# Kernel optimization log

Hardware: AMD Instinct MI355X
Metric: run time of the kernel (lower is better)

Reference implementation:

```python
import jax, jax.numpy as jnp
import numpy as np

TEMPERATURE = 0.07

def _l2norm(x):
    return x / jnp.linalg.norm(x, axis=-1, keepdims=True)

def setup_inputs() -> dict:
    key = jax.random.key(0)
    k1, k2, k3, k4 = jax.random.split(key, 4)
    B, T, C_ctx, C_enc, P, K = 8, 256, 512, 256, 12, 128
    context = jax.random.normal(k1, (B, T, C_ctx), dtype=jnp.float32)
    encoded = jax.random.normal(k2, (B, T, C_enc), dtype=jnp.float32)
    W = jax.random.normal(k3, (P, C_enc, C_ctx), dtype=jnp.float32) * (1.0 / np.sqrt(C_ctx))
    neg_idx = jax.random.randint(k4, (P, B * (T - 1), K), 0, B * T, dtype=jnp.int64)
    return {"context": context, "encoded": encoded, "W": W, "neg_idx": neg_idx}

def reference(context, encoded, W, neg_idx):
    B, T, C_enc = encoded.shape
    n_pred = W.shape[0]
    # normalized pool of all encoded vectors [B*T, C_enc]
    pool = _l2norm(encoded.reshape(B * T, C_enc))
    total = jnp.float32(0.0)
    for k in range(1, n_pred + 1):  # fixed small loop over horizons
        Nk = B * (T - k)
        c_t = context[:, : T - k, :]                       # [B, T-k, C_ctx]
        z_hat = jnp.einsum('btc,ec->bte', c_t, W[k - 1])   # [B, T-k, C_enc]
        z_hat = _l2norm(z_hat.reshape(Nk, C_enc))
        z_pos = _l2norm(encoded[:, k:, :].reshape(Nk, C_enc))
        pos_logits = jnp.sum(z_hat * z_pos, axis=-1, keepdims=True)  # [Nk, 1]
        z_neg = pool[neg_idx[k - 1, :Nk]]                  # [Nk, K, C_enc]
        neg_logits = jnp.einsum('nc,nkc->nk', z_hat, z_neg)
        logits = jnp.concatenate([pos_logits, neg_logits], axis=1) / TEMPERATURE
        # cross-entropy with target class 0
        step_loss = jnp.mean(jax.nn.logsumexp(logits, axis=-1) - logits[:, 0])
        total = total + step_loss
    return total / n_pred
```

## Files before the change

### kernel.cpp

```cpp
#include <hip/hip_runtime.h>
#include <hip/hip_bf16.h>

typedef __attribute__((ext_vector_type(8))) short short8;
typedef __attribute__((ext_vector_type(4))) float f32x4;
typedef _Float16 __attribute__((ext_vector_type(2))) half2v;

#define INV_TEMP 14.285714285714286f
#define LOGIT_MAX 14.2857143f
#define L2E 1.44269504f
#define OFFE (LOGIT_MAX * L2E)
#define PCLIP 0.23f
#define PDELTA (PCLIP / 7.f)
#define PQS (7.f / PCLIP)

__device__ __forceinline__ ushort bf16c(float f) {
  uint u = __float_as_uint(f);
  uint r = (u + 0x7fffu + ((u >> 16) & 1u)) >> 16;
  return (ushort)r;
}
__device__ __forceinline__ uint pk2(float a, float b) {
  return (uint)bf16c(a) | ((uint)bf16c(b) << 16);
}
__device__ __forceinline__ uint pkh(float a, float b) {
  return __builtin_bit_cast(uint, __builtin_amdgcn_cvt_pkrtz(a, b));
}
__device__ __forceinline__ half2v h2(uint u) {
  return __builtin_bit_cast(half2v, u);
}
__device__ __forceinline__ int sdot4_(uint a, uint b, int c) {
  return __builtin_amdgcn_sdot4((int)a, (int)b, c, false);
}
__device__ __forceinline__ void gl_lds16(const void* g, void* l) {
  __builtin_amdgcn_global_load_lds(
      (const __attribute__((address_space(1))) void*)g,
      (__attribute__((address_space(3))) void*)l, 16, 0, 0);
}

template <int CTRL>
__device__ __forceinline__ float dpp_add(float v) {
  const int x = __builtin_amdgcn_mov_dpp(__float_as_int(v), CTRL, 0xF, 0xF, true);
  return v + __int_as_float(x);
}
template <int CTRL>
__device__ __forceinline__ int dpp_addi(int v) {
  return v + __builtin_amdgcn_mov_dpp(v, CTRL, 0xF, 0xF, true);
}
__device__ __forceinline__ float qsum16(float v) {
  v = dpp_add<0xB1>(v);
  v = dpp_add<0x4E>(v);
  v = dpp_add<0x141>(v);
  v = dpp_add<0x140>(v);
  return v;
}
__device__ __forceinline__ int qsum8i(int v) {
  v = dpp_addi<0xB1>(v);
  v = dpp_addi<0x4E>(v);
  v = dpp_addi<0x141>(v);
  return v;
}

__global__ __launch_bounds__(256) void prep_kernel(
    const float* __restrict__ ctx, const float* __restrict__ W,
    const float* __restrict__ enc, ushort* __restrict__ ctxb,
    ushort* __restrict__ Wb, uint* __restrict__ pool4,
    float* __restrict__ acc) {
  const int bid = blockIdx.x;
  const int tid = threadIdx.x;
  if (bid < 1280) {
    const float* in;
    ushort* out;
    size_t i;
    if (bid < 512) { in = ctx; out = ctxb; i = (size_t)bid * 256 + tid; }
    else           { in = W;   out = Wb;   i = (size_t)(bid - 512) * 256 + tid; }
    const float4 a = *(const float4*)(in + i * 8);
    const float4 b = *(const float4*)(in + i * 8 + 4);
    const uint4 o = make_uint4(pk2(a.x, a.y), pk2(a.z, a.w), pk2(b.x, b.y), pk2(b.z, b.w));
    *(uint4*)(out + i * 8) = o;
    return;
  }
  if (bid == 1280 && tid < 12) acc[tid] = 0.f;
  const int grp = tid >> 4, lane = tid & 15;
  const int r = (bid - 1280) * 16 + grp;
  const float* src = enc + (size_t)r * 256 + lane * 16;
  float4 v0 = *(const float4*)(src);
  float4 v1 = *(const float4*)(src + 4);
  float4 v2 = *(const float4*)(src + 8);
  float4 v3 = *(const float4*)(src + 12);
  float c[16] = {v0.x, v0.y, v0.z, v0.w, v1.x, v1.y, v1.z, v1.w,
                 v2.x, v2.y, v2.z, v2.w, v3.x, v3.y, v3.z, v3.w};
  float ss = 0.f;
#pragma unroll
  for (int i = 0; i < 16; ++i) ss = fmaf(c[i], c[i], ss);
  ss = qsum16(ss);
  const float qs = rsqrtf(ss) * PQS;
  uint w0 = 0, w1 = 0;
#pragma unroll
  for (int n = 0; n < 8; ++n) {
    const int q0 = (int)rintf(fminf(fmaxf(c[n] * qs, -7.f), 7.f)) + 8;
    const int q1 = (int)rintf(fminf(fmaxf(c[8 + n] * qs, -7.f), 7.f)) + 8;
    w0 |= (uint)q0 << (4 * n);
    w1 |= (uint)q1 << (4 * n);
  }
  *(uint2*)(pool4 + (size_t)r * 32 + lane * 2) = make_uint2(w0, w1);
}

__global__ __launch_bounds__(256) void zhat_gemm_kernel(
    const ushort* __restrict__ ctxb, const ushort* __restrict__ Wb,
    uint* __restrict__ Zp) {
  const int kk = blockIdx.z;
  const int Tk = 255 - kk, Nk = 8 * Tk;
  const int rowbase = blockIdx.y * 64;
  if (rowbase >= Nk) return;
  const int colbase = blockIdx.x * 128;

  __shared__ __attribute__((aligned(16))) ushort As[64 * 32];
  __shared__ __attribute__((aligned(16))) ushort Bs[128 * 32];

  const int tid = threadIdx.x;
  const int wid = tid >> 6, lane = tid & 63;
  const int arow = tid & 63;
  const int akseg = (tid >> 6) * 8;
  int n = rowbase + arow;
  if (n >= Nk) n = Nk - 1;
  const int bb = n / Tk, tt = n - bb * Tk;
  const ushort* aptr = ctxb + ((size_t)(bb * 256 + tt)) * 512 + akseg;
  const int brow = tid & 127;
  const int bke = (tid >> 7) * 8;
  const ushort* bptr = Wb + ((size_t)kk * 256 + colbase + brow) * 512 + bke;

  char* As_w = (char*)As + wid * 1024;
  char* Bs_w = (char*)Bs + wid * 1024;

  const int wm = wid >> 1, wn = wid & 1;
  const int l15 = lane & 15, l16 = lane >> 4;

  f32x4 acc[2][4];
#pragma unroll
  for (int i = 0; i < 2; ++i)
#pragma unroll
    for (int j = 0; j < 4; ++j) acc[i][j] = (f32x4){0.f, 0.f, 0.f, 0.f};

  const ushort* aread = As + (size_t)(l16 * 64 + wm * 32 + l15) * 8;
  const ushort* bread = Bs + (size_t)(l16 * 128 + wn * 64 + l15) * 8;

  for (int k0 = 0; k0 < 512; k0 += 32) {
    __syncthreads();
    gl_lds16(aptr + k0, As_w);
    gl_lds16(bptr + k0, Bs_w);
    gl_lds16(bptr + k0 + 16, Bs_w + 4096);
    __syncthreads();
    short8 bf[4];
#pragma unroll
    for (int nb = 0; nb < 4; ++nb) bf[nb] = *(const short8*)(bread + (size_t)nb * 16 * 8);
#pragma unroll
    for (int mb = 0; mb < 2; ++mb) {
      short8 af = *(const short8*)(aread + (size_t)mb * 16 * 8);
#pragma unroll
      for (int nb = 0; nb < 4; ++nb)
        acc[mb][nb] = __builtin_amdgcn_mfma_f32_16x16x32_bf16(af, bf[nb], acc[mb][nb], 0, 0, 0);
    }
  }

#pragma unroll
  for (int mb = 0; mb < 2; ++mb) {
    const int row0 = rowbase + wm * 32 + mb * 16 + l16 * 4;
#pragma unroll
    for (int r = 0; r < 4; ++r) {
      const int row = row0 + r;
      if (row < Nk) {
        uint* zp = Zp + ((size_t)kk * 2040 + row) * 128 + (colbase >> 1) + wn * 32 + l15;
        zp[0]  = pkh(acc[mb][0][r], acc[mb][1][r]);
        zp[16] = pkh(acc[mb][2][r], acc[mb][3][r]);
      }
    }
  }
}

#define DOTN(P) ({                                                              \
    int d0_ = 0, d1_ = 0;                                                       \
    uint e_, o_;                                                                \
    e_ = P.x & 0x0F0F0F0Fu; o_ = (P.x >> 4) & 0x0F0F0F0Fu;                      \
    d0_ = sdot4_(zq[0], e_, d0_); d1_ = sdot4_(zq[4], o_, d1_);                 \
    e_ = P.y & 0x0F0F0F0Fu; o_ = (P.y >> 4) & 0x0F0F0F0Fu;                      \
    d0_ = sdot4_(zq[1], e_, d0_); d1_ = sdot4_(zq[5], o_, d1_);                 \
    e_ = P.z & 0x0F0F0F0Fu; o_ = (P.z >> 4) & 0x0F0F0F0Fu;                      \
    d0_ = sdot4_(zq[2], e_, d0_); d1_ = sdot4_(zq[6], o_, d1_);                 \
    e_ = P.w & 0x0F0F0F0Fu; o_ = (P.w >> 4) & 0x0F0F0F0Fu;                      \
    d0_ = sdot4_(zq[3], e_, d0_); d1_ = sdot4_(zq[7], o_, d1_);                 \
    qsum8i(d0_ + d1_); })

#define LDB(P, IDX) P = *(const uint4*)(pbase + (size_t)(uint)(IDX) * 32);
#define ACCB(SUM, P) SUM += exp2f(fmaf((float)DOTN(P), kG, c2m));

__global__ __launch_bounds__(256) void loss_kernel(
    const uint* __restrict__ Zp, const uint* __restrict__ pool4,
    const int* __restrict__ neg_idx, float* __restrict__ acc) {
  const int kk = blockIdx.y;
  const int Tk = 255 - kk, Nk = 8 * Tk;
  if ((int)(blockIdx.x * 16) >= Nk) return;
  const int tid = threadIdx.x;
  const int n = blockIdx.x * 16 + (tid >> 4);
  const int l = tid & 15;
  const int h = l >> 3;
  const int g = l & 7;
  float row_loss = 0.f;
  if (n < Nk) {
    const uint* zr = Zp + ((size_t)kk * 2040 + n) * 128 + g * 16;
    uint zu[16];
#pragma unroll
    for (int i = 0; i < 4; ++i) *(uint4*)(zu + 4 * i) = *(const uint4*)(zr + 4 * i);
    float zf[32];
#pragma unroll
    for (int c = 0; c < 16; ++c) {
      const half2v hv = h2(zu[c]);
      zf[c] = (float)hv.x;
      zf[16 + c] = (float)hv.y;
    }
    float ss = 0.f;
#pragma unroll
    for (int i = 0; i < 32; ++i) ss = fmaf(zf[i], zf[i], ss);
    ss = dpp_add<0xB1>(ss); ss = dpp_add<0x4E>(ss); ss = dpp_add<0x141>(ss);
    const float s127 = rsqrtf(ss) * 127.f;
    uint zq[8];
#pragma unroll
    for (int t = 0; t < 4; ++t) {
      const uint e0 = (uint)((int)rintf(zf[8 * t]     * s127) & 255);
      const uint e1 = (uint)((int)rintf(zf[8 * t + 2] * s127) & 255);
      const uint e2 = (uint)((int)rintf(zf[8 * t + 4] * s127) & 255);
      const uint e3 = (uint)((int)rintf(zf[8 * t + 6] * s127) & 255);
      zq[t] = e0 | (e1 << 8) | (e2 << 16) | (e3 << 24);
      const uint o0 = (uint)((int)rintf(zf[8 * t + 1] * s127) & 255);
      const uint o1 = (uint)((int)rintf(zf[8 * t + 3] * s127) & 255);
      const uint o2 = (uint)((int)rintf(zf[8 * t + 5] * s127) & 255);
      const uint o3 = (uint)((int)rintf(zf[8 * t + 7] * s127) & 255);
      zq[t + 4] = o0 | (o1 << 8) | (o2 << 16) | (o3 << 24);
    }
    int nq = 0, zs = 0;
#pragma unroll
    for (int t = 0; t < 8; ++t) {
      nq = sdot4_(zq[t], zq[t], nq);
      zs = sdot4_(zq[t], 0x01010101u, zs);
    }
    nq = qsum8i(nq);
    zs = qsum8i(zs);
    const float kG = (INV_TEMP * L2E * PDELTA) * rsqrtf((float)nq);
    const float c2 = -8.f * (float)zs * kG;
    const float c2m = c2 - OFFE;

    const uint* pbase = pool4 + g * 4;
    const int bb = n / Tk, tt = n - bb * Tk;
    uint4 PP;
    LDB(PP, bb * 256 + tt + kk + 1)
    const float pose = fmaf((float)DOTN(PP), kG, c2);

    const int* ip = neg_idx + ((size_t)kk * 2040 + n) * 128 + h * 64;
    float s0 = 0.f, s1 = 0.f, s2 = 0.f, s3 = 0.f;
    uint4 A, B, C, D, E, F, G, H;
    {
      const int4 iv = *(const int4*)ip;
      LDB(A, iv.x) LDB(B, iv.y) LDB(C, iv.z) LDB(D, iv.w)
    }
    for (int j8 = 0; j8 < 8; ++j8) {
      {
        const int4 jv = *(const int4*)(ip + j8 * 8 + 4);
        LDB(E, jv.x) LDB(F, jv.y) LDB(G, jv.z) LDB(H, jv.w)
      }
      ACCB(s0, A) ACCB(s1, B) ACCB(s2, C) ACCB(s3, D)
      if (j8 < 7) {
        const int4 kv = *(const int4*)(ip + j8 * 8 + 8);
        LDB(A, kv.x) LDB(B, kv.y) LDB(C, kv.z) LDB(D, kv.w)
      }
      ACCB(s0, E) ACCB(s1, F) ACCB(s2, G) ACCB(s3, H)
    }
    float sl = (s0 + s1) + (s2 + s3);
    sl = dpp_add<0x140>(sl);
    const float ssum = sl + exp2f(pose - OFFE);
    row_loss = LOGIT_MAX + 0.69314718f * (__log2f(ssum) - pose);
  }
  __shared__ float bl[16];
  if (l == 0) bl[tid >> 4] = row_loss;
  __syncthreads();
  if (tid == 0) {
    float s = 0.f;
#pragma unroll
    for (int i = 0; i < 16; ++i) s += bl[i];
    atomicAdd(&acc[kk], s);
  }
}

__global__ void finalize_kernel(const float* __restrict__ acc,
                                float* __restrict__ out) {
  if (threadIdx.x == 0) {
    float tot = 0.f;
#pragma unroll
    for (int kk = 0; kk < 12; ++kk) tot += acc[kk] / (8.0f * (255 - kk));
    out[0] = tot / 12.0f;
  }
}

extern "C" void kernel_launch(void* const* d_in, const int* in_sizes, int n_in,
                              void* d_out, int out_size, void* d_ws, size_t ws_size,
                              hipStream_t stream) {
  const float* ctx = (const float*)d_in[0];
  const float* enc = (const float*)d_in[1];
  const float* W   = (const float*)d_in[2];
  const int*   neg = (const int*)d_in[3];
  float* out = (float*)d_out;

  char* ws = (char*)d_ws;
  uint*   pool4 = (uint*)(ws);
  ushort* ctxb  = (ushort*)(ws + 262144);
  ushort* Wb    = (ushort*)(ws + 2359296);
  uint*   Zp    = (uint*)(ws + 5505024);
  float*  accb  = (float*)(ws + 18038784);

  prep_kernel<<<dim3(1408), dim3(256), 0, stream>>>(ctx, W, enc, ctxb, Wb, pool4, accb);
  zhat_gemm_kernel<<<dim3(2, 32, 12), dim3(256), 0, stream>>>(ctxb, Wb, Zp);
  loss_kernel<<<dim3(128, 12), dim3(256), 0, stream>>>(Zp, pool4, neg, accb);
  finalize_kernel<<<dim3(1), dim3(64), 0, stream>>>(accb, out);
}
```

Baseline: 66.36 us.

## Double-buffer LDS tiles in z_hat GEMM to overlap loads with MFMA

The z_hat GEMM K-loop now uses two LDS buffers for the A and B tiles. The next K-slice is issued with direct global-to-LDS loads while MFMAs run on the current slice, and the two barriers per step become one explicit waitcnt plus barrier. This is meant to hide global load latency behind compute, at the cost of twice the shared memory per block, which may reduce occupancy.

Result: no change. 66.44 us (+0.1%).

```diff
diff --git a/kernel.cpp b/kernel.cpp
--- a/kernel.cpp
+++ b/kernel.cpp
@@ -113,26 +113,22 @@
   if (rowbase >= Nk) return;
   const int colbase = blockIdx.x * 128;
 
-  __shared__ __attribute__((aligned(16))) ushort As[64 * 32];
-  __shared__ __attribute__((aligned(16))) ushort Bs[128 * 32];
+  __shared__ __attribute__((aligned(16))) ushort As[2][64 * 32];
+  __shared__ __attribute__((aligned(16))) ushort Bs[2][128 * 32];
 
   const int tid = threadIdx.x;
   const int wid = tid >> 6, lane = tid & 63;
   const int arow = tid & 63;
-  const int akseg = (tid >> 6) * 8;
   int n = rowbase + arow;
   if (n >= Nk) n = Nk - 1;
   const int bb = n / Tk, tt = n - bb * Tk;
-  const ushort* aptr = ctxb + ((size_t)(bb * 256 + tt)) * 512 + akseg;
+  const ushort* aptr = ctxb + ((size_t)(bb * 256 + tt)) * 512 + (tid >> 6) * 8;
   const int brow = tid & 127;
-  const int bke = (tid >> 7) * 8;
-  const ushort* bptr = Wb + ((size_t)kk * 256 + colbase + brow) * 512 + bke;
-
-  char* As_w = (char*)As + wid * 1024;
-  char* Bs_w = (char*)Bs + wid * 1024;
+  const ushort* bptr = Wb + ((size_t)kk * 256 + colbase + brow) * 512 + (tid >> 7) * 8;
 
   const int wm = wid >> 1, wn = wid & 1;
   const int l15 = lane & 15, l16 = lane >> 4;
+  const int wboff = wid * 1024;
 
   f32x4 acc[2][4];
 #pragma unroll
@@ -140,26 +136,50 @@
 #pragma unroll
     for (int j = 0; j < 4; ++j) acc[i][j] = (f32x4){0.f, 0.f, 0.f, 0.f};
 
-  const ushort* aread = As + (size_t)(l16 * 64 + wm * 32 + l15) * 8;
-  const ushort* bread = Bs + (size_t)(l16 * 128 + wn * 64 + l15) * 8;
-
-  for (int k0 = 0; k0 < 512; k0 += 32) {
-    __syncthreads();
-    gl_lds16(aptr + k0, As_w);
-    gl_lds16(bptr + k0, Bs_w);
-    gl_lds16(bptr + k0 + 16, Bs_w + 4096);
-    __syncthreads();
-    short8 bf[4];
-#pragma unroll
-    for (int nb = 0; nb < 4; ++nb) bf[nb] = *(const short8*)(bread + (size_t)nb * 16 * 8);
-#pragma unroll
-    for (int mb = 0; mb < 2; ++mb) {
-      short8 af = *(const short8*)(aread + (size_t)mb * 16 * 8);
-#pragma unroll
-      for (int nb = 0; nb < 4; ++nb)
-        acc[mb][nb] = __builtin_amdgcn_mfma_f32_16x16x32_bf16(af, bf[nb], acc[mb][nb], 0, 0, 0);
-    }
-  }
+  const size_t aoff = (size_t)(l16 * 64 + wm * 32 + l15) * 8;
+  const size_t boff = (size_t)(l16 * 128 + wn * 64 + l15) * 8;
+
+#define STAGE(B, K0)                                              \
+  gl_lds16(aptr + (K0), (char*)As[B] + wboff);                    \
+  gl_lds16(bptr + (K0), (char*)Bs[B] + wboff);                    \
+  gl_lds16(bptr + (K0) + 16, (char*)Bs[B] + wboff + 4096);
+
+#define SYNCPT                                                    \
+  asm volatile("s_waitcnt vmcnt(0)" ::: "memory");                \
+  __builtin_amdgcn_s_barrier();                                   \
+  __builtin_amdgcn_sched_barrier(0);
+
+#define COMPUTE(B)                                                              \
+  {                                                                             \
+    const ushort* ar = As[B] + aoff;                                            \
+    const ushort* br = Bs[B] + boff;                                            \
+    short8 bf[4];                                                               \
+    bf[0] = *(const short8*)(br);                                               \
+    bf[1] = *(const short8*)(br + 128);                                         \
+    bf[2] = *(const short8*)(br + 256);                                         \
+    bf[3] = *(const short8*)(br + 384);                                         \
+    const short8 a0 = *(const short8*)(ar);                                     \
+    const short8 a1 = *(const short8*)(ar + 128);                               \
+    _Pragma("unroll")                                                           \
+    for (int nb = 0; nb < 4; ++nb) {                                            \
+      acc[0][nb] = __builtin_amdgcn_mfma_f32_16x16x32_bf16(a0, bf[nb], acc[0][nb], 0, 0, 0); \
+      acc[1][nb] = __builtin_amdgcn_mfma_f32_16x16x32_bf16(a1, bf[nb], acc[1][nb], 0, 0, 0); \
+    }                                                                           \
+  }
+
+  STAGE(0, 0)
+  SYNCPT
+  for (int k0 = 0; k0 < 512; k0 += 64) {
+    STAGE(1, k0 + 32)
+    COMPUTE(0)
+    SYNCPT
+    if (k0 + 64 < 512) { STAGE(0, k0 + 64) }
+    COMPUTE(1)
+    SYNCPT
+  }
+#undef STAGE
+#undef SYNCPT
+#undef COMPUTE
 
 #pragma unroll
   for (int mb = 0; mb < 2; ++mb) {
```
